# Optimization experiments

Hardware: AMD Instinct MI355X
Metric: run time of the kernel (lower is better)

## Reference

```python
import jax, jax.numpy as jnp
import numpy as np

B, T, C, HS = 8, 2048, 768, 256  # batch, seq(block_size), n_embed, head_size


def setup_inputs() -> dict:
    key = jax.random.key(0)
    kx, kq, kk, kv = jax.random.split(key, 4)
    scale = 1.0 / np.sqrt(C)
    return {
        "x": jax.random.normal(kx, (B, T, C), dtype=jnp.float32),
        # torch nn.Linear(n_embed, head_size, bias=False) computes x @ W.T;
        # store weights pre-transposed as [in, out].
        "Wq": jax.random.normal(kq, (C, HS), dtype=jnp.float32) * scale,
        "Wk": jax.random.normal(kk, (C, HS), dtype=jnp.float32) * scale,
        "Wv": jax.random.normal(kv, (C, HS), dtype=jnp.float32) * scale,
    }


def reference(x, Wq, Wk, Wv):
    Bx, Tx, Cx = x.shape
    q = x @ Wq  # [B,T,HS]
    k = x @ Wk  # [B,T,HS]
    v = x @ Wv  # [B,T,HS]
    # NOTE: original scales by C**-0.5 with C = n_embed (not head_size)
    att = jnp.einsum('btd,bsd->bts', q, k) * (Cx ** -0.5)  # [B,T,T]
    causal = jnp.tril(jnp.ones((Tx, Tx), dtype=bool))
    att = jnp.where(causal, att, -jnp.inf)
    probs = jax.nn.softmax(att, axis=-1)
    # dropout=0.0 -> identity (eval mode)
    out = jnp.einsum('bts,bsd->btd', probs, v)  # [B,T,HS]
    return out
```

## Files before the change

kernel.cpp:

```cpp
#include <hip/hip_runtime.h>
#include <hip/hip_bf16.h>
#include <math.h>

#define B_  8
#define T_  2048
#define C_  768
#define HS_ 256

#define CHUNK_TILES 4
#define CHUNKS_PER_BATCH 72
#define NPART (CHUNKS_PER_BATCH * B_)

typedef float  f32x4  __attribute__((ext_vector_type(4)));
typedef __bf16 bf16x8 __attribute__((ext_vector_type(8)));
typedef __bf16 bf16x4 __attribute__((ext_vector_type(4)));

#define MFMA16(a, b, c) __builtin_amdgcn_mfma_f32_16x16x32_bf16((a), (b), (c), 0, 0, 0)

#define GLOAD_LDS16(gp, lp)                                                     \
    __builtin_amdgcn_global_load_lds(                                           \
        (const __attribute__((address_space(1))) void*)(gp),                    \
        (__attribute__((address_space(3))) void*)(lp), 16, 0, 0)

__device__ __forceinline__ int chunk_cum128(int qb) {
    int p = qb >> 1;
    return p * (p + 1) + (qb & 1) * (p + 1);
}

__global__ __launch_bounds__(256) void xb_kernel(const float* __restrict__ x,
                                                 __bf16* __restrict__ xb) {
    size_t i = ((size_t)blockIdx.x * 256 + threadIdx.x) * 8;
    f32x4 a = *(const f32x4*)(x + i);
    f32x4 b = *(const f32x4*)(x + i + 4);
    bf16x8 o;
    o[0] = (__bf16)a[0]; o[1] = (__bf16)a[1]; o[2] = (__bf16)a[2]; o[3] = (__bf16)a[3];
    o[4] = (__bf16)b[0]; o[5] = (__bf16)b[1]; o[6] = (__bf16)b[2]; o[7] = (__bf16)b[3];
    *(bf16x8*)(xb + i) = o;
}

__global__ __launch_bounds__(256) void wt_kernel(const float* __restrict__ Wq,
                                                 const float* __restrict__ Wk,
                                                 const float* __restrict__ Wv,
                                                 __bf16* __restrict__ wt_all,
                                                 float qscale) {
    int idx = blockIdx.x * 256 + threadIdx.x;
    int mat = blockIdx.y;
    const float* W = (mat == 0) ? Wq : ((mat == 1) ? Wk : Wv);
    float scale = (mat == 0) ? qscale : 1.0f;
    int k = idx >> 8;
    int n = idx & 255;
    wt_all[((size_t)mat * HS_ + n) * C_ + k] = (__bf16)(W[idx] * scale);
}

__global__ __launch_bounds__(256) void proj_kernel(const __bf16* __restrict__ xb,
                                                   const __bf16* __restrict__ wt,
                                                   __bf16* __restrict__ qf_,
                                                   __bf16* __restrict__ kf_,
                                                   __bf16* __restrict__ vf_) {
    __shared__ alignas(16) __bf16 ldsA[128 * 64];
    __shared__ alignas(16) __bf16 ldsB[128 * 64];

    const int tid  = threadIdx.x;
    const int w    = tid >> 6;
    const int lane = tid & 63;
    const int cm   = lane & 15;
    const int quad = lane >> 4;
    const int wm   = w & 1;
    const int wn   = w >> 1;
    const int m0   = blockIdx.x * 128;
    const int n0   = blockIdx.y * 128;

    f32x4 acc[4][4];
#pragma unroll
    for (int i = 0; i < 4; i++)
#pragma unroll
        for (int j = 0; j < 4; j++) acc[i][j] = (f32x4){0.f, 0.f, 0.f, 0.f};

    for (int k0 = 0; k0 < C_; k0 += 64) {
        __syncthreads();
#pragma unroll
        for (int h = 0; h < 4; h++) {
            int c = tid + h * 256;
            GLOAD_LDS16(xb + (size_t)(m0 + (c >> 3)) * C_ + k0 + (c & 7) * 8,
                        ldsA + c * 8);
        }
#pragma unroll
        for (int h = 0; h < 4; h++) {
            int c = tid + h * 256;
            GLOAD_LDS16(wt + (size_t)(n0 + (c >> 3)) * C_ + k0 + (c & 7) * 8,
                        ldsB + c * 8);
        }
        __syncthreads();

#pragma unroll
        for (int ks = 0; ks < 2; ks++) {
            bf16x8 af[4], bfr[4];
#pragma unroll
            for (int mt = 0; mt < 4; mt++)
                af[mt] = *(const bf16x8*)&ldsA[(wm * 64 + mt * 16 + cm) * 64 + ks * 32 + quad * 8];
#pragma unroll
            for (int nt = 0; nt < 4; nt++)
                bfr[nt] = *(const bf16x8*)&ldsB[(wn * 64 + nt * 16 + cm) * 64 + ks * 32 + quad * 8];
#pragma unroll
            for (int mt = 0; mt < 4; mt++)
#pragma unroll
                for (int nt = 0; nt < 4; nt++)
                    acc[mt][nt] = MFMA16(af[mt], bfr[nt], acc[mt][nt]);
        }
    }

    const int mat   = n0 >> 8;
    const int dBase = (n0 & 255) + wn * 64;
    const int b     = m0 >> 11;
    const int rt    = ((m0 & 2047) + wm * 64) >> 6;

    if (mat == 0) {
#pragma unroll
        for (int mt = 0; mt < 4; mt++)
#pragma unroll
            for (int nt = 0; nt < 4; nt++) {
                int ksq   = (dBase >> 5) + (nt >> 1);
                int quad2 = (nt & 1) * 2 + (cm >> 3);
                int j     = cm & 7;
                size_t base = ((((size_t)(b * 32 + rt) * 4 + mt) * 8 + ksq) * 64
                               + quad2 * 16) * 8 + j;
#pragma unroll
                for (int i = 0; i < 4; i++)
                    qf_[base + (quad * 4 + i) * 8] = (__bf16)acc[mt][nt][i];
            }
    } else if (mat == 1) {
#pragma unroll
        for (int mt = 0; mt < 4; mt++)
#pragma unroll
            for (int nt = 0; nt < 4; nt++) {
                int ksq   = (dBase >> 5) + (nt >> 1);
                int quad2 = (nt & 1) * 2 + (cm >> 3);
                int j     = cm & 7;
                size_t base = ((((size_t)(b * 32 + rt) * 8 + ksq) * 4 + mt) * 64
                               + quad2 * 16) * 8 + j;
#pragma unroll
                for (int i = 0; i < 4; i++)
                    kf_[base + (quad * 4 + i) * 8] = (__bf16)acc[mt][nt][i];
            }
    } else {
#pragma unroll
        for (int mt = 0; mt < 4; mt++) {
            int ks2   = (mt >> 1) & 1;
            int quadF = (mt & 1) * 2 + (quad >> 1);
            int jb    = (quad & 1) * 4;
#pragma unroll
            for (int nt = 0; nt < 4; nt++) {
                int ntv = (dBase >> 4) + nt;
                size_t idx = ((((size_t)(b * 32 + rt) * 2 + ks2) * 16 + ntv) * 64
                              + quadF * 16 + cm) * 8 + jb;
                bf16x4 v4;
                v4[0] = (__bf16)acc[mt][nt][0]; v4[1] = (__bf16)acc[mt][nt][1];
                v4[2] = (__bf16)acc[mt][nt][2]; v4[3] = (__bf16)acc[mt][nt][3];
                *(bf16x4*)(vf_ + idx) = v4;
            }
        }
    }
}

__global__ __launch_bounds__(512) void flash_part(const __bf16* __restrict__ qf_,
                                                  const __bf16* __restrict__ kf_,
                                                  const __bf16* __restrict__ vf_,
                                                  __bf16* __restrict__ Opart,
                                                  float* __restrict__ mpart,
                                                  float* __restrict__ lpart) {
    __shared__ alignas(16) __bf16 ldsK[2][8 * 4 * 64 * 8];
    __shared__ alignas(16) __bf16 ldsV[2][2 * 16 * 64 * 8];
    __shared__ alignas(16) __bf16 ldsPw[8][1024];

    const int tid  = threadIdx.x;
    const int w    = tid >> 6;
    const int lane = tid & 63;
    const int cm   = lane & 15;
    const int quad = lane >> 4;

    const int pid = blockIdx.x;
    const int b   = pid & 7;
    const int r   = (CHUNKS_PER_BATCH - 1) - (pid >> 3);
    int qb = 0, ci = 0;
    {
        int rr = r;
        for (int j = 0; j < 16; j++) {
            int c = (j >> 1) + 1;
            if (rr < c) { qb = j; ci = rr; break; }
            rr -= c;
        }
    }
    const int lpid = b * CHUNKS_PER_BATCH + r;
    const int kt_begin = ci * CHUNK_TILES;
    const int kt_end   = min(kt_begin + CHUNK_TILES, 2 * qb + 2);
    const int ntile    = kt_end - kt_begin;

    const int qt = 2 * qb + (w >> 2);
    const __bf16* qp = qf_ + (((size_t)(b * 32 + qt) * 4 + (w & 3)) * 8) * 512 + lane * 8;
    bf16x8 qf[8];
#pragma unroll
    for (int ks = 0; ks < 8; ks++) qf[ks] = *(const bf16x8*)(qp + ks * 512);

    f32x4 accO[16];
#pragma unroll
    for (int i = 0; i < 16; i++) accO[i] = (f32x4){0.f, 0.f, 0.f, 0.f};
    float mi[4], li[4];
#pragma unroll
    for (int i = 0; i < 4; i++) { mi[i] = -__builtin_inff(); li[i] = 0.f; }

    const int wrow = qb * 128 + w * 16;
    const int qg   = wrow + quad * 4;

    {
        const __bf16* kg = kf_ + ((size_t)(b * 32 + kt_begin) * 8) * 2048;
        const __bf16* vg = vf_ + ((size_t)(b * 32 + kt_begin) * 2) * 8192;
#pragma unroll
        for (int h = 0; h < 4; h++) {
            GLOAD_LDS16(kg + (size_t)(h * 512 + tid) * 8, ldsK[0] + (h * 512 + w * 64) * 8);
            GLOAD_LDS16(vg + (size_t)(h * 512 + tid) * 8, ldsV[0] + (h * 512 + w * 64) * 8);
        }
    }

    for (int it = 0; it < ntile; it++) {
        const int kt  = kt_begin + it;
        const int cur = it & 1;

        __syncthreads();

        if (it + 1 < ntile) {
            const __bf16* kg = kf_ + ((size_t)(b * 32 + kt + 1) * 8) * 2048;
            const __bf16* vg = vf_ + ((size_t)(b * 32 + kt + 1) * 2) * 8192;
#pragma unroll
            for (int h = 0; h < 4; h++) {
                GLOAD_LDS16(kg + (size_t)(h * 512 + tid) * 8,
                            ldsK[cur ^ 1] + (h * 512 + w * 64) * 8);
                GLOAD_LDS16(vg + (size_t)(h * 512 + tid) * 8,
                            ldsV[cur ^ 1] + (h * 512 + w * 64) * 8);
            }
        }

        f32x4 s[4];
#pragma unroll
        for (int i = 0; i < 4; i++) s[i] = (f32x4){0.f, 0.f, 0.f, 0.f};
#pragma unroll
        for (int nsub = 0; nsub < 4; nsub++) {
#pragma unroll
            for (int ks = 0; ks < 8; ks++) {
                bf16x8 kfr = *(const bf16x8*)&ldsK[cur][ks * 2048 + nsub * 512 + lane * 8];
                s[nsub] = MFMA16(qf[ks], kfr, s[nsub]);
            }
        }
        if (kt * 64 + 63 > wrow) {
#pragma unroll
            for (int nsub = 0; nsub < 4; nsub++)
#pragma unroll
                for (int i = 0; i < 4; i++)
                    if (kt * 64 + nsub * 16 + cm > qg + i)
                        s[nsub][i] = -__builtin_inff();
        }
        float pm[4];
#pragma unroll
        for (int i = 0; i < 4; i++)
            pm[i] = fmaxf(fmaxf(s[0][i], s[1][i]), fmaxf(s[2][i], s[3][i]));
#pragma unroll
        for (int off = 1; off < 16; off <<= 1)
#pragma unroll
            for (int i = 0; i < 4; i++)
                pm[i] = fmaxf(pm[i], __shfl_xor(pm[i], off));

        float alpha[4], rs[4], p[4][4];
#pragma unroll
        for (int i = 0; i < 4; i++) {
            float mn = fmaxf(mi[i], pm[i]);
            alpha[i] = exp2f(mi[i] - mn);
            mi[i] = mn;
            rs[i] = 0.f;
        }
#pragma unroll
        for (int nsub = 0; nsub < 4; nsub++)
#pragma unroll
            for (int i = 0; i < 4; i++) {
                p[nsub][i] = exp2f(s[nsub][i] - mi[i]);
                rs[i] += p[nsub][i];
            }
#pragma unroll
        for (int off = 1; off < 16; off <<= 1)
#pragma unroll
            for (int i = 0; i < 4; i++)
                rs[i] += __shfl_xor(rs[i], off);
#pragma unroll
        for (int i = 0; i < 4; i++) li[i] = li[i] * alpha[i] + rs[i];
#pragma unroll
        for (int nt = 0; nt < 16; nt++)
#pragma unroll
            for (int i = 0; i < 4; i++) accO[nt][i] *= alpha[i];

        __bf16* ldsP = ldsPw[w];
#pragma unroll
        for (int nsub = 0; nsub < 4; nsub++)
#pragma unroll
            for (int i = 0; i < 4; i++) {
                int c = nsub * 16 + cm;
                ldsP[(c >> 5) * 512 + ((c >> 3) & 3) * 128 + (quad * 4 + i) * 8 + (c & 7)]
                    = (__bf16)p[nsub][i];
            }
#pragma unroll
        for (int ks2 = 0; ks2 < 2; ks2++) {
            bf16x8 pf = *(const bf16x8*)&ldsP[ks2 * 512 + quad * 128 + cm * 8];
#pragma unroll
            for (int nt = 0; nt < 16; nt++) {
                bf16x8 vfr = *(const bf16x8*)&ldsV[cur][ks2 * 8192 + nt * 512 + lane * 8];
                accO[nt] = MFMA16(pf, vfr, accO[nt]);
            }
        }
    }

    const int rloc = w * 16 + quad * 4;
    __bf16* op = Opart + ((size_t)lpid * 128 + rloc) * HS_;
#pragma unroll
    for (int nt = 0; nt < 16; nt++)
#pragma unroll
        for (int i = 0; i < 4; i++)
            op[(size_t)i * HS_ + nt * 16 + cm] = (__bf16)accO[nt][i];
    if (cm == 0) {
#pragma unroll
        for (int i = 0; i < 4; i++) {
            mpart[lpid * 128 + rloc + i] = mi[i];
            lpart[lpid * 128 + rloc + i] = li[i];
        }
    }
}

__global__ __launch_bounds__(256) void flash_combine(const __bf16* __restrict__ Opart,
                                                     const float* __restrict__ mpart,
                                                     const float* __restrict__ lpart,
                                                     float* __restrict__ out) {
    const int b    = blockIdx.x >> 4;
    const int qb   = blockIdx.x & 15;
    const int nc   = (qb >> 1) + 1;
    const int pid0 = b * CHUNKS_PER_BATCH + chunk_cum128(qb);

    const int tid  = threadIdx.x;
    const int col  = (tid & 63) * 4;
    const int r0   = blockIdx.y * 16 + (tid >> 6) * 4;

    for (int rr = 0; rr < 4; rr++) {
        const int row = r0 + rr;
        float ms = -__builtin_inff();
        for (int c = 0; c < nc; c++)
            ms = fmaxf(ms, mpart[(pid0 + c) * 128 + row]);
        f32x4 acc = (f32x4){0.f, 0.f, 0.f, 0.f};
        float l = 0.f;
        for (int c = 0; c < nc; c++) {
            float sc = exp2f(mpart[(pid0 + c) * 128 + row] - ms);
            l += lpart[(pid0 + c) * 128 + row] * sc;
            bf16x4 o = *(const bf16x4*)(Opart + ((size_t)(pid0 + c) * 128 + row) * HS_ + col);
            acc[0] += (float)o[0] * sc; acc[1] += (float)o[1] * sc;
            acc[2] += (float)o[2] * sc; acc[3] += (float)o[3] * sc;
        }
        float inv = 1.0f / l;
        f32x4 res = (f32x4){acc[0] * inv, acc[1] * inv, acc[2] * inv, acc[3] * inv};
        *(f32x4*)(out + ((size_t)(b * T_ + qb * 128 + row)) * HS_ + col) = res;
    }
}

extern "C" void kernel_launch(void* const* d_in, const int* in_sizes, int n_in,
                              void* d_out, int out_size, void* d_ws, size_t ws_size,
                              hipStream_t stream) {
    const float* x  = (const float*)d_in[0];
    const float* Wq = (const float*)d_in[1];
    const float* Wk = (const float*)d_in[2];
    const float* Wv = (const float*)d_in[3];
    float* out = (float*)d_out;

    char* ws = (char*)d_ws;
    size_t off = 0;
    __bf16* wt_all = (__bf16*)(ws + off); off += 1179648;
    __bf16* qfrag  = (__bf16*)(ws + off); off += 8388608;
    __bf16* kfrag  = (__bf16*)(ws + off); off += 8388608;
    __bf16* vfrag  = (__bf16*)(ws + off); off += 8388608;
    __bf16* xb     = (__bf16*)(ws + off);
    __bf16* Opart  = (__bf16*)(ws + off); off += (size_t)NPART * 128 * HS_ * 2;
    float*  mpart  = (float*)(ws + off);  off += (size_t)NPART * 128 * 4;
    float*  lpart  = (float*)(ws + off);

    float qscale = 1.4426950408889634f / sqrtf((float)C_);

    xb_kernel<<<dim3(6144), 256, 0, stream>>>(x, xb);
    wt_kernel<<<dim3(768, 3), 256, 0, stream>>>(Wq, Wk, Wv, wt_all, qscale);
    proj_kernel<<<dim3(128, 6), 256, 0, stream>>>(xb, wt_all, qfrag, kfrag, vfrag);
    flash_part<<<dim3(NPART), 512, 0, stream>>>(qfrag, kfrag, vfrag, Opart, mpart, lpart);
    flash_combine<<<dim3(128, 8), 256, 0, stream>>>(Opart, mpart, lpart, out);
}
```

Measured before the change: 212.1 us.

## Retile flash attention to 64-row query blocks with 32-key tiles and transposed S

Shrinks each flash_part workgroup from 128 query rows and 8 waves to 64 rows and 4 waves, with 32-key tiles and chunks of up to 8 tiles. This doubles the partition count to fill more CUs. S is computed transposed (K as the A operand), so each lane owns a single query row, which reduces the softmax reductions to two shuffles. The accumulator rescale is skipped when no row max changed. Double-buffered async LDS prefetch is replaced by single-buffered loads with an extra barrier, which exposes load latency. The combine kernel is adapted with vectorized m/l loads.

```diff
diff --git a/kernel.cpp b/kernel.cpp
--- a/kernel.cpp
+++ b/kernel.cpp
@@ -7,13 +7,13 @@
 #define C_  768
 #define HS_ 256
 
-#define CHUNK_TILES 4
-#define CHUNKS_PER_BATCH 72
-#define NPART (CHUNKS_PER_BATCH * B_)
+#define CHUNKS_PER_BATCH 144
+#define NSLOT (CHUNKS_PER_BATCH * B_)
 
 typedef float  f32x4  __attribute__((ext_vector_type(4)));
 typedef __bf16 bf16x8 __attribute__((ext_vector_type(8)));
 typedef __bf16 bf16x4 __attribute__((ext_vector_type(4)));
+typedef __bf16 bf16x2 __attribute__((ext_vector_type(2)));
 
 #define MFMA16(a, b, c) __builtin_amdgcn_mfma_f32_16x16x32_bf16((a), (b), (c), 0, 0, 0)
 
@@ -22,9 +22,9 @@
         (const __attribute__((address_space(1))) void*)(gp),                    \
         (__attribute__((address_space(3))) void*)(lp), 16, 0, 0)
 
-__device__ __forceinline__ int chunk_cum128(int qb) {
-    int p = qb >> 1;
-    return p * (p + 1) + (qb & 1) * (p + 1);
+__device__ __forceinline__ int chunk_cum64(int qb) {
+    int g = qb >> 2;
+    return 2 * g * (g + 1) + (qb & 3) * (g + 1);
 }
 
 __global__ __launch_bounds__(256) void xb_kernel(const float* __restrict__ x,
@@ -162,15 +162,15 @@
     }
 }
 
-__global__ __launch_bounds__(512) void flash_part(const __bf16* __restrict__ qf_,
+__global__ __launch_bounds__(256) void flash_part(const __bf16* __restrict__ qf_,
                                                   const __bf16* __restrict__ kf_,
                                                   const __bf16* __restrict__ vf_,
                                                   __bf16* __restrict__ Opart,
                                                   float* __restrict__ mpart,
                                                   float* __restrict__ lpart) {
-    __shared__ alignas(16) __bf16 ldsK[2][8 * 4 * 64 * 8];
-    __shared__ alignas(16) __bf16 ldsV[2][2 * 16 * 64 * 8];
-    __shared__ alignas(16) __bf16 ldsPw[8][1024];
+    __shared__ alignas(16) __bf16 ldsK[8 * 2 * 64 * 8];
+    __shared__ alignas(16) __bf16 ldsV[16 * 64 * 8];
+    __shared__ alignas(16) __bf16 ldsP[4][512];
 
     const int tid  = threadIdx.x;
     const int w    = tid >> 6;
@@ -178,25 +178,23 @@
     const int cm   = lane & 15;
     const int quad = lane >> 4;
 
-    const int pid = blockIdx.x;
-    const int b   = pid & 7;
-    const int r   = (CHUNKS_PER_BATCH - 1) - (pid >> 3);
+    const int pid  = blockIdx.x;
+    const int b    = pid & 7;
+    const int r    = (CHUNKS_PER_BATCH - 1) - (pid >> 3);
     int qb = 0, ci = 0;
     {
         int rr = r;
-        for (int j = 0; j < 16; j++) {
-            int c = (j >> 1) + 1;
+        for (int j = 0; j < 32; j++) {
+            int c = (j >> 2) + 1;
             if (rr < c) { qb = j; ci = rr; break; }
             rr -= c;
         }
     }
     const int lpid = b * CHUNKS_PER_BATCH + r;
-    const int kt_begin = ci * CHUNK_TILES;
-    const int kt_end   = min(kt_begin + CHUNK_TILES, 2 * qb + 2);
-    const int ntile    = kt_end - kt_begin;
-
-    const int qt = 2 * qb + (w >> 2);
-    const __bf16* qp = qf_ + (((size_t)(b * 32 + qt) * 4 + (w & 3)) * 8) * 512 + lane * 8;
+    const int kt_begin = ci * 8;
+    const int kt_end   = min(kt_begin + 8, 2 * qb + 2);
+
+    const __bf16* qp = qf_ + (((size_t)(b * 32 + qb) * 4 + w) * 8) * 512 + lane * 8;
     bf16x8 qf[8];
 #pragma unroll
     for (int ks = 0; ks < 8; ks++) qf[ks] = *(const bf16x8*)(qp + ks * 512);
@@ -204,130 +202,113 @@
     f32x4 accO[16];
 #pragma unroll
     for (int i = 0; i < 16; i++) accO[i] = (f32x4){0.f, 0.f, 0.f, 0.f};
-    float mi[4], li[4];
-#pragma unroll
-    for (int i = 0; i < 4; i++) { mi[i] = -__builtin_inff(); li[i] = 0.f; }
-
-    const int wrow = qb * 128 + w * 16;
-    const int qg   = wrow + quad * 4;
-
-    {
-        const __bf16* kg = kf_ + ((size_t)(b * 32 + kt_begin) * 8) * 2048;
-        const __bf16* vg = vf_ + ((size_t)(b * 32 + kt_begin) * 2) * 8192;
-#pragma unroll
-        for (int h = 0; h < 4; h++) {
-            GLOAD_LDS16(kg + (size_t)(h * 512 + tid) * 8, ldsK[0] + (h * 512 + w * 64) * 8);
-            GLOAD_LDS16(vg + (size_t)(h * 512 + tid) * 8, ldsV[0] + (h * 512 + w * 64) * 8);
-        }
-    }
-
-    for (int it = 0; it < ntile; it++) {
-        const int kt  = kt_begin + it;
-        const int cur = it & 1;
-
+    float mi = -__builtin_inff(), li = 0.f;
+
+    const int wrow  = qb * 64 + w * 16;
+    const int qglob = wrow + cm;
+
+    for (int kt = kt_begin; kt < kt_end; kt++) {
         __syncthreads();
 
-        if (it + 1 < ntile) {
-            const __bf16* kg = kf_ + ((size_t)(b * 32 + kt + 1) * 8) * 2048;
-            const __bf16* vg = vf_ + ((size_t)(b * 32 + kt + 1) * 2) * 8192;
+        {
+            const int kt64 = kt >> 1, kh = kt & 1;
+            const __bf16* kgb = kf_ + (((size_t)(b * 32 + kt64) * 8) * 4 + kh * 2) * 512;
 #pragma unroll
             for (int h = 0; h < 4; h++) {
-                GLOAD_LDS16(kg + (size_t)(h * 512 + tid) * 8,
-                            ldsK[cur ^ 1] + (h * 512 + w * 64) * 8);
-                GLOAD_LDS16(vg + (size_t)(h * 512 + tid) * 8,
-                            ldsV[cur ^ 1] + (h * 512 + w * 64) * 8);
-            }
-        }
-
-        f32x4 s[4];
-#pragma unroll
-        for (int i = 0; i < 4; i++) s[i] = (f32x4){0.f, 0.f, 0.f, 0.f};
-#pragma unroll
-        for (int nsub = 0; nsub < 4; nsub++) {
+                int g = h * 256 + tid;
+                int ks = g >> 7, sub = g & 127;
+                GLOAD_LDS16(kgb + (size_t)ks * 4 * 512 + sub * 8,
+                            ldsK + (h * 256 + w * 64) * 8);
+            }
+            const __bf16* vgb = vf_ + ((size_t)(b * 64 + kt) * 16) * 512;
+#pragma unroll
+            for (int h = 0; h < 4; h++) {
+                int g = h * 256 + tid;
+                GLOAD_LDS16(vgb + (size_t)g * 8,
+                            ldsV + (h * 256 + w * 64) * 8);
+            }
+        }
+        __syncthreads();
+
+        f32x4 s[2];
+#pragma unroll
+        for (int i = 0; i < 2; i++) s[i] = (f32x4){0.f, 0.f, 0.f, 0.f};
+#pragma unroll
+        for (int ns = 0; ns < 2; ns++)
 #pragma unroll
             for (int ks = 0; ks < 8; ks++) {
-                bf16x8 kfr = *(const bf16x8*)&ldsK[cur][ks * 2048 + nsub * 512 + lane * 8];
-                s[nsub] = MFMA16(qf[ks], kfr, s[nsub]);
-            }
-        }
-        if (kt * 64 + 63 > wrow) {
-#pragma unroll
-            for (int nsub = 0; nsub < 4; nsub++)
+                bf16x8 kfr = *(const bf16x8*)&ldsK[(ks * 2 + ns) * 512 + lane * 8];
+                s[ns] = MFMA16(kfr, qf[ks], s[ns]);
+            }
+        if (kt * 32 + 31 > wrow) {
+#pragma unroll
+            for (int ns = 0; ns < 2; ns++)
 #pragma unroll
                 for (int i = 0; i < 4; i++)
-                    if (kt * 64 + nsub * 16 + cm > qg + i)
-                        s[nsub][i] = -__builtin_inff();
-        }
-        float pm[4];
+                    if (kt * 32 + ns * 16 + quad * 4 + i > qglob)
+                        s[ns][i] = -__builtin_inff();
+        }
+        float pm = -__builtin_inff();
+#pragma unroll
+        for (int ns = 0; ns < 2; ns++)
+#pragma unroll
+            for (int i = 0; i < 4; i++) pm = fmaxf(pm, s[ns][i]);
+        pm = fmaxf(pm, __shfl_xor(pm, 16));
+        pm = fmaxf(pm, __shfl_xor(pm, 32));
+
+        float mn = fmaxf(mi, pm);
+        float al = exp2f(mi - mn);
+        mi = mn;
+        float p[2][4], rs = 0.f;
+#pragma unroll
+        for (int ns = 0; ns < 2; ns++)
+#pragma unroll
+            for (int i = 0; i < 4; i++) {
+                p[ns][i] = exp2f(s[ns][i] - mn);
+                rs += p[ns][i];
+            }
+        rs += __shfl_xor(rs, 16);
+        rs += __shfl_xor(rs, 32);
+        li = li * al + rs;
+
+        if (__any(al != 1.0f)) {
+            float aa[4];
+#pragma unroll
+            for (int i = 0; i < 4; i++) aa[i] = __shfl(al, quad * 4 + i);
+#pragma unroll
+            for (int nt = 0; nt < 16; nt++)
+#pragma unroll
+                for (int i = 0; i < 4; i++) accO[nt][i] *= aa[i];
+        }
+
+#pragma unroll
+        for (int ns = 0; ns < 2; ns++)
+#pragma unroll
+            for (int i2 = 0; i2 < 2; i2++) {
+                bf16x2 d2;
+                d2[0] = (__bf16)p[ns][2 * i2];
+                d2[1] = (__bf16)p[ns][2 * i2 + 1];
+                int off = ((ns * 2 + (quad >> 1)) * 16 + cm) * 8
+                          + (quad & 1) * 4 + i2 * 2;
+                *(bf16x2*)&ldsP[w][off] = d2;
+            }
+        bf16x8 pfrag = *(const bf16x8*)&ldsP[w][(quad * 16 + cm) * 8];
+#pragma unroll
+        for (int nt = 0; nt < 16; nt++) {
+            bf16x8 vfr = *(const bf16x8*)&ldsV[(nt * 64 + lane) * 8];
+            accO[nt] = MFMA16(pfrag, vfr, accO[nt]);
+        }
+    }
+
+#pragma unroll
+    for (int nt = 0; nt < 16; nt++)
 #pragma unroll
         for (int i = 0; i < 4; i++)
-            pm[i] = fmaxf(fmaxf(s[0][i], s[1][i]), fmaxf(s[2][i], s[3][i]));
-#pragma unroll
-        for (int off = 1; off < 16; off <<= 1)
-#pragma unroll
-            for (int i = 0; i < 4; i++)
-                pm[i] = fmaxf(pm[i], __shfl_xor(pm[i], off));
-
-        float alpha[4], rs[4], p[4][4];
-#pragma unroll
-        for (int i = 0; i < 4; i++) {
-            float mn = fmaxf(mi[i], pm[i]);
-            alpha[i] = exp2f(mi[i] - mn);
-            mi[i] = mn;
-            rs[i] = 0.f;
-        }
-#pragma unroll
-        for (int nsub = 0; nsub < 4; nsub++)
-#pragma unroll
-            for (int i = 0; i < 4; i++) {
-                p[nsub][i] = exp2f(s[nsub][i] - mi[i]);
-                rs[i] += p[nsub][i];
-            }
-#pragma unroll
-        for (int off = 1; off < 16; off <<= 1)
-#pragma unroll
-            for (int i = 0; i < 4; i++)
-                rs[i] += __shfl_xor(rs[i], off);
-#pragma unroll
-        for (int i = 0; i < 4; i++) li[i] = li[i] * alpha[i] + rs[i];
-#pragma unroll
-        for (int nt = 0; nt < 16; nt++)
-#pragma unroll
-            for (int i = 0; i < 4; i++) accO[nt][i] *= alpha[i];
-
-        __bf16* ldsP = ldsPw[w];
-#pragma unroll
-        for (int nsub = 0; nsub < 4; nsub++)
-#pragma unroll
-            for (int i = 0; i < 4; i++) {
-                int c = nsub * 16 + cm;
-                ldsP[(c >> 5) * 512 + ((c >> 3) & 3) * 128 + (quad * 4 + i) * 8 + (c & 7)]
-                    = (__bf16)p[nsub][i];
-            }
-#pragma unroll
-        for (int ks2 = 0; ks2 < 2; ks2++) {
-            bf16x8 pf = *(const bf16x8*)&ldsP[ks2 * 512 + quad * 128 + cm * 8];
-#pragma unroll
-            for (int nt = 0; nt < 16; nt++) {
-                bf16x8 vfr = *(const bf16x8*)&ldsV[cur][ks2 * 8192 + nt * 512 + lane * 8];
-                accO[nt] = MFMA16(pf, vfr, accO[nt]);
-            }
-        }
-    }
-
-    const int rloc = w * 16 + quad * 4;
-    __bf16* op = Opart + ((size_t)lpid * 128 + rloc) * HS_;
-#pragma unroll
-    for (int nt = 0; nt < 16; nt++)
-#pragma unroll
-        for (int i = 0; i < 4; i++)
-            op[(size_t)i * HS_ + nt * 16 + cm] = (__bf16)accO[nt][i];
-    if (cm == 0) {
-#pragma unroll
-        for (int i = 0; i < 4; i++) {
-            mpart[lpid * 128 + rloc + i] = mi[i];
-            lpart[lpid * 128 + rloc + i] = li[i];
-        }
+            Opart[((size_t)lpid * 64 + w * 16 + quad * 4 + i) * HS_ + nt * 16 + cm]
+                = (__bf16)accO[nt][i];
+    if (quad == 0) {
+        mpart[lpid * 64 + w * 16 + cm] = mi;
+        lpart[lpid * 64 + w * 16 + cm] = li;
     }
 }
 
@@ -335,32 +316,45 @@
                                                      const float* __restrict__ mpart,
                                                      const float* __restrict__ lpart,
                                                      float* __restrict__ out) {
-    const int b    = blockIdx.x >> 4;
-    const int qb   = blockIdx.x & 15;
-    const int nc   = (qb >> 1) + 1;
-    const int pid0 = b * CHUNKS_PER_BATCH + chunk_cum128(qb);
+    const int b    = blockIdx.x >> 5;
+    const int qb   = blockIdx.x & 31;
+    const int nc   = (qb >> 2) + 1;
+    const int pid0 = b * CHUNKS_PER_BATCH + chunk_cum64(qb);
 
     const int tid  = threadIdx.x;
     const int col  = (tid & 63) * 4;
     const int r0   = blockIdx.y * 16 + (tid >> 6) * 4;
 
-    for (int rr = 0; rr < 4; rr++) {
-        const int row = r0 + rr;
-        float ms = -__builtin_inff();
-        for (int c = 0; c < nc; c++)
-            ms = fmaxf(ms, mpart[(pid0 + c) * 128 + row]);
-        f32x4 acc = (f32x4){0.f, 0.f, 0.f, 0.f};
-        float l = 0.f;
-        for (int c = 0; c < nc; c++) {
-            float sc = exp2f(mpart[(pid0 + c) * 128 + row] - ms);
-            l += lpart[(pid0 + c) * 128 + row] * sc;
-            bf16x4 o = *(const bf16x4*)(Opart + ((size_t)(pid0 + c) * 128 + row) * HS_ + col);
-            acc[0] += (float)o[0] * sc; acc[1] += (float)o[1] * sc;
-            acc[2] += (float)o[2] * sc; acc[3] += (float)o[3] * sc;
-        }
-        float inv = 1.0f / l;
-        f32x4 res = (f32x4){acc[0] * inv, acc[1] * inv, acc[2] * inv, acc[3] * inv};
-        *(f32x4*)(out + ((size_t)(b * T_ + qb * 128 + row)) * HS_ + col) = res;
+    f32x4 ms = (f32x4){-__builtin_inff(), -__builtin_inff(),
+                       -__builtin_inff(), -__builtin_inff()};
+    for (int c = 0; c < nc; c++) {
+        f32x4 m4 = *(const f32x4*)(mpart + (pid0 + c) * 64 + r0);
+#pragma unroll
+        for (int i = 0; i < 4; i++) ms[i] = fmaxf(ms[i], m4[i]);
+    }
+    f32x4 acc[4];
+#pragma unroll
+    for (int i = 0; i < 4; i++) acc[i] = (f32x4){0.f, 0.f, 0.f, 0.f};
+    f32x4 lt = (f32x4){0.f, 0.f, 0.f, 0.f};
+    for (int c = 0; c < nc; c++) {
+        f32x4 m4 = *(const f32x4*)(mpart + (pid0 + c) * 64 + r0);
+        f32x4 l4 = *(const f32x4*)(lpart + (pid0 + c) * 64 + r0);
+#pragma unroll
+        for (int i = 0; i < 4; i++) {
+            float sc = exp2f(m4[i] - ms[i]);
+            lt[i] += l4[i] * sc;
+            bf16x4 o = *(const bf16x4*)(Opart
+                        + ((size_t)(pid0 + c) * 64 + r0 + i) * HS_ + col);
+            acc[i][0] += (float)o[0] * sc; acc[i][1] += (float)o[1] * sc;
+            acc[i][2] += (float)o[2] * sc; acc[i][3] += (float)o[3] * sc;
+        }
+    }
+#pragma unroll
+    for (int i = 0; i < 4; i++) {
+        float inv = 1.0f / lt[i];
+        f32x4 res = (f32x4){acc[i][0] * inv, acc[i][1] * inv,
+                            acc[i][2] * inv, acc[i][3] * inv};
+        *(f32x4*)(out + ((size_t)(b * T_ + qb * 64 + r0 + i)) * HS_ + col) = res;
     }
 }
 
@@ -380,8 +374,8 @@
     __bf16* kfrag  = (__bf16*)(ws + off); off += 8388608;
     __bf16* vfrag  = (__bf16*)(ws + off); off += 8388608;
     __bf16* xb     = (__bf16*)(ws + off);
-    __bf16* Opart  = (__bf16*)(ws + off); off += (size_t)NPART * 128 * HS_ * 2;
-    float*  mpart  = (float*)(ws + off);  off += (size_t)NPART * 128 * 4;
+    __bf16* Opart  = (__bf16*)(ws + off); off += (size_t)NSLOT * 64 * HS_ * 2;
+    float*  mpart  = (float*)(ws + off);  off += (size_t)NSLOT * 64 * 4;
     float*  lpart  = (float*)(ws + off);
 
     float qscale = 1.4426950408889634f / sqrtf((float)C_);
@@ -389,6 +383,6 @@
     xb_kernel<<<dim3(6144), 256, 0, stream>>>(x, xb);
     wt_kernel<<<dim3(768, 3), 256, 0, stream>>>(Wq, Wk, Wv, wt_all, qscale);
     proj_kernel<<<dim3(128, 6), 256, 0, stream>>>(xb, wt_all, qfrag, kfrag, vfrag);
-    flash_part<<<dim3(NPART), 512, 0, stream>>>(qfrag, kfrag, vfrag, Opart, mpart, lpart);
-    flash_combine<<<dim3(128, 8), 256, 0, stream>>>(Opart, mpart, lpart, out);
-}
+    flash_part<<<dim3(NSLOT), 256, 0, stream>>>(qfrag, kfrag, vfrag, Opart, mpart, lpart);
+    flash_combine<<<dim3(256, 4), 256, 0, stream>>>(Opart, mpart, lpart, out);
+}
```

After: 202.1 us. 1.05x faster.
